# Performance work log

Hardware: AMD Instinct MI355X
Metric: run time of the kernel (lower is better)

The kernel has to match this reference:

```python
import jax, jax.numpy as jnp
import numpy as np

LEAKY_SLOPE = 0.01  # torch nn.LeakyReLU default


def leaky_relu(x):
    return jnp.where(x >= 0, x, LEAKY_SLOPE * x)


def rgcn_conv(x, edge_index, edge_type, w_rel, w_root, b_conv):
    # PyG RGCNConv: out = x @ W_root + b + sum_r mean_{edges of rel r into i}(x_src @ W_r)
    n = x.shape[0]
    src, dst = edge_index[0], edge_index[1]
    out = x @ w_root + b_conv
    num_rel = w_rel.shape[0]
    for r in range(num_rel):  # small fixed relation count
        mask = (edge_type == r)
        msg = x[src] @ w_rel[r]                      # [E, H]
        msg = jnp.where(mask[:, None], msg, 0.0)
        agg = jax.ops.segment_sum(msg, dst, num_segments=n)          # [N, H]
        cnt = jax.ops.segment_sum(mask.astype(x.dtype), dst, num_segments=n)
        out = out + agg / jnp.maximum(cnt, 1.0)[:, None]             # mean aggr
    return out


def setup_inputs() -> dict:
    key = jax.random.key(0)
    ks = jax.random.split(key, 10)
    N, E, D_IN, H, OUT, R = 50000, 600000, 768, 128, 3, 2
    s_in = 1.0 / np.sqrt(D_IN)
    s_h = 1.0 / np.sqrt(H)
    return {
        "feature": jax.random.normal(ks[0], (N, D_IN), dtype=jnp.float32),
        "edge_index": jax.random.randint(ks[1], (2, E), 0, N, dtype=jnp.int64),
        "edge_type": jax.random.randint(ks[2], (E,), 0, R, dtype=jnp.int64),
        "w_in": jax.random.uniform(ks[3], (D_IN, H), jnp.float32, -s_in, s_in),
        "b_in": jax.random.uniform(ks[4], (H,), jnp.float32, -s_in, s_in),
        "w_rel": jax.random.uniform(ks[5], (R, H, H), jnp.float32, -s_h, s_h),
        "w_root": jax.random.uniform(ks[6], (H, H), jnp.float32, -s_h, s_h),
        "b_conv": jnp.zeros((H,), jnp.float32),
        "w_out": jax.random.uniform(ks[7], (H, OUT), jnp.float32, -s_h, s_h),
        "b_out": jax.random.uniform(ks[8], (OUT,), jnp.float32, -s_h, s_h),
    }


def reference(feature, edge_index, edge_type, w_in, b_in, w_rel, w_root, b_conv, w_out, b_out):
    x = leaky_relu(feature @ w_in + b_in)
    # NOTE: original forward applies rgcn1 twice (shared weights); dropout is
    # identity at inference; rgcn2/linear_relu_output1 are unused.
    x = rgcn_conv(x, edge_index, edge_type, w_rel, w_root, b_conv)
    x = rgcn_conv(x, edge_index, edge_type, w_rel, w_root, b_conv)
    return x @ w_out + b_out
```

## Files before the change

### kernel.cpp

```cpp
#include <hip/hip_runtime.h>

#define H 128
#define CAP 64

typedef _Float16 f16x8 __attribute__((ext_vector_type(8)));
typedef _Float16 f16x4 __attribute__((ext_vector_type(4)));
typedef float    f32x4 __attribute__((ext_vector_type(4)));

__global__ __launch_bounds__(256) void hist_fill(const int* __restrict__ src,
    const int* __restrict__ dst, const int* __restrict__ et,
    int* __restrict__ cnt, int* __restrict__ elist, int E, int N)
{
    int e = blockIdx.x * 256 + threadIdx.x;
    if (e >= E) return;
    int s = src[e], d = dst[e], t = et[e];
    int b = t * N + d;
    int pos = atomicAdd(&cnt[b], 1);
    if (pos < CAP) elist[(size_t)b * CAP + pos] = s;
}

__global__ __launch_bounds__(256) void prep_w(const float* __restrict__ w_in,
    const float* __restrict__ w_root, const float* __restrict__ w_rel,
    _Float16* __restrict__ wInT, _Float16* __restrict__ wcatT, int K)
{
    int idx = blockIdx.x * 256 + threadIdx.x;
    int tot1 = K * H;
    if (idx < tot1) {
        int k = idx >> 7, c = idx & 127;
        int o = ((k >> 3) << 10) + (c << 3) + (k & 7);
        wInT[o] = (_Float16)w_in[idx];
    } else {
        int i2 = idx - tot1;
        if (i2 < H * 384) {
            int c = i2 / 384, k = i2 - c * 384;
            float v;
            if (k < 128)      v = w_root[(size_t)k * H + c];
            else if (k < 256) v = w_rel[(size_t)(k - 128) * H + c];
            else              v = w_rel[(size_t)H * H + (size_t)(k - 256) * H + c];
            wcatT[i2] = (_Float16)v;
        }
    }
}

__global__ __launch_bounds__(256) void prep_fin(const float* __restrict__ w_root,
    const float* __restrict__ w_rel, const float* __restrict__ b_conv,
    const float* __restrict__ w_out, const float* __restrict__ b_out,
    float* __restrict__ wfin, float* __restrict__ bfin, int OUT)
{
    int idx = blockIdx.x * 256 + threadIdx.x;
    if (idx < 3 * H) {
        int m = idx >> 7, k = idx & 127;
        const float* W = (m == 0) ? w_root : (w_rel + (size_t)(m - 1) * H * H);
        for (int c = 0; c < OUT; c++) {
            float s = 0.f;
            for (int j = 0; j < H; j++) s += W[(size_t)k * H + j] * w_out[(size_t)j * OUT + c];
            wfin[((size_t)m * H + k) * OUT + c] = s;
        }
    } else if (idx < 3 * H + OUT) {
        int c = idx - 3 * H;
        float s = b_out[c];
        for (int j = 0; j < H; j++) s += b_conv[j] * w_out[(size_t)j * OUT + c];
        bfin[c] = s;
    }
}

__global__ __launch_bounds__(256, 3) void gemm_big(const float* __restrict__ A,
    const _Float16* __restrict__ WP, const float* __restrict__ bias,
    _Float16* __restrict__ C16, int M, int K, int ldc)
{
    __shared__ _Float16 As[2][8192];

    const int tid = threadIdx.x;
    const int w   = tid >> 6;
    const int l   = tid & 63;
    const int l15 = l & 15;
    const int q   = l >> 4;
    const int brow = blockIdx.x * 64;
    const int wr   = w * 16;

    const int srow = wr + (l >> 5);
    const int sk4  = (l & 31) * 4;
    const int slot = (l & 31) >> 1;
    const int half = l & 1;

    const _Float16* bp = WP + ((size_t)q * H + l15) * 8;

    float bj[8];
#pragma unroll
    for (int j = 0; j < 8; j++) bj[j] = bias[j * 16 + l15];

    f32x4 acc[8];
    const f32x4 z4 = {0.f, 0.f, 0.f, 0.f};
#pragma unroll
    for (int j = 0; j < 8; j++) acc[j] = z4;

    const int chunks = K / 128;
    float4 st[8];

    {
        const float* apc = A + sk4;
#pragma unroll
        for (int i = 0; i < 8; i++) {
            int gr = brow + srow + i * 2; if (gr >= M) gr = M - 1;
            st[i] = *(const float4*)(apc + (size_t)gr * K);
        }
#pragma unroll
        for (int i = 0; i < 8; i++) {
            int row = srow + i * 2;
            int idx = slot * 512 + ((row ^ (slot & 7)) << 3) + half * 4;
            f16x4 v; v[0] = (_Float16)st[i].x; v[1] = (_Float16)st[i].y;
                     v[2] = (_Float16)st[i].z; v[3] = (_Float16)st[i].w;
            *(f16x4*)&As[0][idx] = v;
        }
    }
    __syncthreads();

    for (int c = 0; c < chunks; c++) {
        const bool more = (c + 1) < chunks;
        if (more) {
            const float* apc = A + (c + 1) * 128 + sk4;
#pragma unroll
            for (int i = 0; i < 8; i++) {
                int gr = brow + srow + i * 2; if (gr >= M) gr = M - 1;
                st[i] = *(const float4*)(apc + (size_t)gr * K);
            }
        }
        {
            const _Float16* __restrict__ buf = As[c & 1];
#pragma unroll
            for (int ks = 0; ks < 4; ks++) {
                const int sl = ks * 4 + q;
                f16x8 af = *(const f16x8*)&buf[sl * 512 + (((wr + l15) ^ (sl & 7)) << 3)];
                const _Float16* bks = bp + (size_t)(c * 4 + ks) * 4096;
                f16x8 bf[8];
#pragma unroll
                for (int j = 0; j < 8; j++) bf[j] = *(const f16x8*)(bks + j * 128);
#pragma unroll
                for (int j = 0; j < 8; j++)
                    acc[j] = __builtin_amdgcn_mfma_f32_16x16x32_f16(af, bf[j], acc[j], 0, 0, 0);
            }
        }
        if (more) {
            _Float16* __restrict__ buf = As[(c + 1) & 1];
#pragma unroll
            for (int i = 0; i < 8; i++) {
                int row = srow + i * 2;
                int idx = slot * 512 + ((row ^ (slot & 7)) << 3) + half * 4;
                f16x4 v; v[0] = (_Float16)st[i].x; v[1] = (_Float16)st[i].y;
                         v[2] = (_Float16)st[i].z; v[3] = (_Float16)st[i].w;
                *(f16x4*)&buf[idx] = v;
            }
        }
        __syncthreads();
    }

#pragma unroll
    for (int rg = 0; rg < 4; rg++) {
        int row = brow + wr + q * 4 + rg;
        if (row < M) {
#pragma unroll
            for (int j = 0; j < 8; j++) {
                float v = acc[j][rg] + bj[j];
                v = (v >= 0.f) ? v : 0.01f * v;
                C16[(size_t)row * ldc + j * 16 + l15] = (_Float16)v;
            }
        }
    }
}

template<int MODE>
__global__ __launch_bounds__(256) void gather_k(const _Float16* __restrict__ X,
    int ldx, _Float16* __restrict__ Mout, const int* __restrict__ elist,
    const int* __restrict__ cnt, int N,
    const float* __restrict__ wfin, const float* __restrict__ bfin,
    float* __restrict__ out)
{
    int wv = blockIdx.x * 4 + (threadIdx.x >> 6);
    int l  = threadIdx.x & 63;
    if (wv >= N) return;

    const int eo   = l >> 4;
    const int e2   = eo & 1;
    const int half = l >> 5;
    const int c8   = (l & 15) * 8;

    int dr = cnt[(size_t)half * N + wv];
    int d  = dr < CAP ? dr : CAP;
    float inv = dr > 0 ? 1.f / (float)dr : 0.f;
    const int* lst = elist + ((size_t)half * N + wv) * CAP;

    float acc[8];
#pragma unroll
    for (int j = 0; j < 8; j++) acc[j] = 0.f;

    const f16x8 zv = {};
    for (int p = e2; p < d; p += 8) {
        int p1 = p + 2, p2 = p + 4, p3 = p + 6;
        int s0 = lst[p];
        f16x8 v0 = *(const f16x8*)&X[(size_t)s0 * ldx + c8];
        f16x8 v1 = zv, v2 = zv, v3 = zv;
        if (p1 < d) { int s = lst[p1]; v1 = *(const f16x8*)&X[(size_t)s * ldx + c8]; }
        if (p2 < d) { int s = lst[p2]; v2 = *(const f16x8*)&X[(size_t)s * ldx + c8]; }
        if (p3 < d) { int s = lst[p3]; v3 = *(const f16x8*)&X[(size_t)s * ldx + c8]; }
#pragma unroll
        for (int j = 0; j < 8; j++)
            acc[j] += (float)v0[j] + (float)v1[j] + (float)v2[j] + (float)v3[j];
    }

#pragma unroll
    for (int j = 0; j < 8; j++) {
        acc[j] += __shfl_xor(acc[j], 16);
        acc[j] *= inv;
    }

    if (MODE == 0) {
        if (eo == 0) {
            f16x8 o;
#pragma unroll
            for (int j = 0; j < 8; j++) o[j] = (_Float16)acc[j];
            *(f16x8*)&Mout[(size_t)wv * 384 + 128 + c8] = o;
        } else if (eo == 2) {
            f16x8 o;
#pragma unroll
            for (int j = 0; j < 8; j++) o[j] = (_Float16)acc[j];
            *(f16x8*)&Mout[(size_t)wv * 384 + 256 + c8] = o;
        }
    } else {
        float p0 = 0.f, p1 = 0.f, p2 = 0.f;
        if (eo == 1) {
            f16x8 xv = *(const f16x8*)&X[(size_t)wv * ldx + c8];
#pragma unroll
            for (int j = 0; j < 8; j++) {
                float xf = (float)xv[j];
                const float* wr = wfin + (size_t)(c8 + j) * 3;
                p0 += xf * wr[0]; p1 += xf * wr[1]; p2 += xf * wr[2];
            }
        } else if (eo == 0 || eo == 2) {
            const float* wb = wfin + (size_t)(eo == 0 ? 1 : 2) * H * 3;
#pragma unroll
            for (int j = 0; j < 8; j++) {
                const float* wr = wb + (size_t)(c8 + j) * 3;
                p0 += acc[j] * wr[0]; p1 += acc[j] * wr[1]; p2 += acc[j] * wr[2];
            }
        }
#pragma unroll
        for (int off = 1; off <= 32; off <<= 1) {
            p0 += __shfl_xor(p0, off);
            p1 += __shfl_xor(p1, off);
            p2 += __shfl_xor(p2, off);
        }
        if (l == 0) {
            out[(size_t)wv * 3 + 0] = p0 + bfin[0];
            out[(size_t)wv * 3 + 1] = p1 + bfin[1];
            out[(size_t)wv * 3 + 2] = p2 + bfin[2];
        }
    }
}

__global__ __launch_bounds__(512) void gemm_cat(const _Float16* __restrict__ XC,
    const _Float16* __restrict__ WT, const float* __restrict__ bias,
    _Float16* __restrict__ X2, int M, int mtiles, int ldc)
{
    const int w   = threadIdx.x >> 6;
    const int l   = threadIdx.x & 63;
    const int l15 = l & 15;
    const int q   = l >> 4;
    const int col = w * 16 + l15;

    f16x8 bf[12];
    {
        const _Float16* wpp = WT + (size_t)col * 384 + q * 8;
#pragma unroll
        for (int c = 0; c < 12; c++) bf[c] = *(const f16x8*)(wpp + c * 32);
    }
    const float bj = bias[col];

    int t = blockIdx.x;
    if (t >= mtiles) return;
    f16x8 xf[12];
    {
        const _Float16* xp = XC + ((size_t)t * 16 + l15) * 384 + q * 8;
#pragma unroll
        for (int c = 0; c < 12; c++) xf[c] = *(const f16x8*)(xp + c * 32);
    }

    const f32x4 z4 = {0.f, 0.f, 0.f, 0.f};
    while (true) {
        int tn = t + gridDim.x;
        bool more = tn < mtiles;
        f16x8 xnf[12];
        if (more) {
            const _Float16* xp = XC + ((size_t)tn * 16 + l15) * 384 + q * 8;
#pragma unroll
            for (int c = 0; c < 12; c++) xnf[c] = *(const f16x8*)(xp + c * 32);
        }

        f32x4 a0 = z4;
#pragma unroll
        for (int c = 0; c < 12; c++)
            a0 = __builtin_amdgcn_mfma_f32_16x16x32_f16(xf[c], bf[c], a0, 0, 0, 0);

#pragma unroll
        for (int rg = 0; rg < 4; rg++) {
            int row = t * 16 + q * 4 + rg;
            if (row < M) X2[(size_t)row * ldc + col] = (_Float16)(a0[rg] + bj);
        }
        if (!more) break;
        t = tn;
#pragma unroll
        for (int c = 0; c < 12; c++) xf[c] = xnf[c];
    }
}

__global__ __launch_bounds__(256) void proj_generic(const _Float16* __restrict__ XC,
    const float* __restrict__ wfin, const float* __restrict__ bfin,
    float* __restrict__ out, int N, int OUT)
{
    int row = blockIdx.x * 4 + (threadIdx.x >> 6);
    int l = threadIdx.x & 63;
    if (row >= N) return;
    float xv[6];
#pragma unroll
    for (int i = 0; i < 6; i++) xv[i] = (float)XC[(size_t)row * 384 + l * 6 + i];
    for (int c = 0; c < OUT; c++) {
        float p = 0.f;
#pragma unroll
        for (int i = 0; i < 6; i++) p += xv[i] * wfin[(size_t)(l * 6 + i) * OUT + c];
        for (int off = 32; off > 0; off >>= 1) p += __shfl_down(p, off);
        if (l == 0) out[(size_t)row * OUT + c] = p + bfin[c];
    }
}

extern "C" void kernel_launch(void* const* d_in, const int* in_sizes, int n_in,
                              void* d_out, int out_size, void* d_ws, size_t ws_size,
                              hipStream_t stream) {
    const float* feature = (const float*)d_in[0];
    const int*   ei      = (const int*)d_in[1];
    const int*   et      = (const int*)d_in[2];
    const float* w_in    = (const float*)d_in[3];
    const float* b_in    = (const float*)d_in[4];
    const float* w_rel   = (const float*)d_in[5];
    const float* w_root  = (const float*)d_in[6];
    const float* b_conv  = (const float*)d_in[7];
    const float* w_out   = (const float*)d_in[8];
    const float* b_out   = (const float*)d_in[9];

    const int HH   = in_sizes[4];
    const int D_IN = in_sizes[3] / HH;
    const int N    = in_sizes[0] / D_IN;
    const int E    = in_sizes[1] / 2;
    const int OUT  = in_sizes[9];

    char* base = (char*)d_ws;
    _Float16* wInT  = (_Float16*)base;
    _Float16* wcatT = wInT + (size_t)D_IN * HH;
    _Float16* xc1   = wcatT + (size_t)HH * 384;
    _Float16* xc2   = xc1 + (size_t)N * 384;
    float* wfin     = (float*)(xc2 + (size_t)N * 384);
    float* bfin     = wfin + (size_t)3 * HH * (OUT > 0 ? OUT : 1);
    int* cnt        = (int*)(bfin + ((OUT + 3) & ~3));
    int* elist      = cnt + (size_t)2 * N;

    hipMemsetAsync(cnt, 0, sizeof(int) * (size_t)2 * N, stream);
    prep_w<<<(D_IN * HH + HH * 384 + 255) / 256, 256, 0, stream>>>(
        w_in, w_root, w_rel, wInT, wcatT, D_IN);
    prep_fin<<<2, 256, 0, stream>>>(w_root, w_rel, b_conv, w_out, b_out,
                                    wfin, bfin, OUT);
    hist_fill<<<(E + 255) / 256, 256, 0, stream>>>(ei, ei + E, et, cnt, elist, E, N);

    gemm_big<<<(N + 63) / 64, 256, 0, stream>>>(feature, wInT, b_in, xc1, N, D_IN, 384);

    const int mtiles  = (N + 15) / 16;
    const int gblocks = (N + 3) / 4;

    gather_k<0><<<gblocks, 256, 0, stream>>>(xc1, 384, xc1, elist, cnt, N,
                                             nullptr, nullptr, nullptr);
    if (OUT == 3) {
        gemm_cat<<<1024, 512, 0, stream>>>(xc1, wcatT, b_conv, xc2, N, mtiles, 128);
        gather_k<1><<<gblocks, 256, 0, stream>>>(xc2, 128, nullptr, elist, cnt, N,
                                                 wfin, bfin, (float*)d_out);
    } else {
        gemm_cat<<<1024, 512, 0, stream>>>(xc1, wcatT, b_conv, xc2, N, mtiles, 384);
        gather_k<0><<<gblocks, 256, 0, stream>>>(xc2, 384, xc2, elist, cnt, N,
                                                 nullptr, nullptr, nullptr);
        proj_generic<<<gblocks, 256, 0, stream>>>(xc2, wfin, bfin, (float*)d_out, N, OUT);
    }
}
```

Before: 449.2 us.

## Pre-convert features to fp16 and split concat buffer into separate arrays

Adds a standalone kernel that converts the fp32 feature matrix to fp16 so the input GEMM loads half-precision tiles directly with simpler staging. The 384-wide concatenated activation buffer is split into an N×128 node array and an N×256 aggregated-message array, with gemm_cat and the gather kernels updated to match. prep_fin is parallelised across output columns. The extra conversion pass adds a full read and write of the feature matrix, which may outweigh the savings in the GEMM's load path.

```diff
diff --git a/kernel.cpp b/kernel.cpp
--- a/kernel.cpp
+++ b/kernel.cpp
@@ -17,6 +17,23 @@
     int b = t * N + d;
     int pos = atomicAdd(&cnt[b], 1);
     if (pos < CAP) elist[(size_t)b * CAP + pos] = s;
+}
+
+__global__ __launch_bounds__(256) void cvt_feat(const float* __restrict__ A,
+    _Float16* __restrict__ A16, long long total8)
+{
+    long long i = (long long)blockIdx.x * 256 + threadIdx.x;
+    long long stride = (long long)gridDim.x * 256;
+    for (; i < total8; i += stride) {
+        float4 v0 = *(const float4*)(A + i * 8);
+        float4 v1 = *(const float4*)(A + i * 8 + 4);
+        f16x8 o;
+        o[0] = (_Float16)v0.x; o[1] = (_Float16)v0.y;
+        o[2] = (_Float16)v0.z; o[3] = (_Float16)v0.w;
+        o[4] = (_Float16)v1.x; o[5] = (_Float16)v1.y;
+        o[6] = (_Float16)v1.z; o[7] = (_Float16)v1.w;
+        *(f16x8*)(A16 + i * 8) = o;
+    }
 }
 
 __global__ __launch_bounds__(256) void prep_w(const float* __restrict__ w_in,
@@ -48,23 +65,24 @@
     float* __restrict__ wfin, float* __restrict__ bfin, int OUT)
 {
     int idx = blockIdx.x * 256 + threadIdx.x;
-    if (idx < 3 * H) {
-        int m = idx >> 7, k = idx & 127;
+    int nw = 3 * H * OUT;
+    if (idx < nw) {
+        int mk = idx / OUT, c = idx - mk * OUT;
+        int m = mk >> 7, k = mk & 127;
         const float* W = (m == 0) ? w_root : (w_rel + (size_t)(m - 1) * H * H);
-        for (int c = 0; c < OUT; c++) {
-            float s = 0.f;
-            for (int j = 0; j < H; j++) s += W[(size_t)k * H + j] * w_out[(size_t)j * OUT + c];
-            wfin[((size_t)m * H + k) * OUT + c] = s;
-        }
-    } else if (idx < 3 * H + OUT) {
-        int c = idx - 3 * H;
+        float s = 0.f;
+        for (int j = 0; j < H; j++)
+            s += W[(size_t)k * H + j] * w_out[(size_t)j * OUT + c];
+        wfin[(size_t)mk * OUT + c] = s;
+    } else if (idx < nw + OUT) {
+        int c = idx - nw;
         float s = b_out[c];
         for (int j = 0; j < H; j++) s += b_conv[j] * w_out[(size_t)j * OUT + c];
         bfin[c] = s;
     }
 }
 
-__global__ __launch_bounds__(256, 3) void gemm_big(const float* __restrict__ A,
+__global__ __launch_bounds__(256, 3) void gemm_big(const _Float16* __restrict__ A16,
     const _Float16* __restrict__ WP, const float* __restrict__ bias,
     _Float16* __restrict__ C16, int M, int K, int ldc)
 {
@@ -78,10 +96,8 @@
     const int brow = blockIdx.x * 64;
     const int wr   = w * 16;
 
-    const int srow = wr + (l >> 5);
-    const int sk4  = (l & 31) * 4;
-    const int slot = (l & 31) >> 1;
-    const int half = l & 1;
+    const int r4  = l >> 4;
+    const int c16 = l & 15;
 
     const _Float16* bp = WP + ((size_t)q * H + l15) * 8;
 
@@ -95,22 +111,19 @@
     for (int j = 0; j < 8; j++) acc[j] = z4;
 
     const int chunks = K / 128;
-    float4 st[8];
+    f16x8 st[4];
 
     {
-        const float* apc = A + sk4;
-#pragma unroll
-        for (int i = 0; i < 8; i++) {
-            int gr = brow + srow + i * 2; if (gr >= M) gr = M - 1;
-            st[i] = *(const float4*)(apc + (size_t)gr * K);
-        }
-#pragma unroll
-        for (int i = 0; i < 8; i++) {
-            int row = srow + i * 2;
-            int idx = slot * 512 + ((row ^ (slot & 7)) << 3) + half * 4;
-            f16x4 v; v[0] = (_Float16)st[i].x; v[1] = (_Float16)st[i].y;
-                     v[2] = (_Float16)st[i].z; v[3] = (_Float16)st[i].w;
-            *(f16x4*)&As[0][idx] = v;
+        const _Float16* apc = A16 + c16 * 8;
+#pragma unroll
+        for (int i = 0; i < 4; i++) {
+            int gr = brow + wr + r4 + i * 4; if (gr >= M) gr = M - 1;
+            st[i] = *(const f16x8*)(apc + (size_t)gr * K);
+        }
+#pragma unroll
+        for (int i = 0; i < 4; i++) {
+            int row = wr + r4 + i * 4;
+            *(f16x8*)&As[0][c16 * 512 + ((row ^ (c16 & 7)) << 3)] = st[i];
         }
     }
     __syncthreads();
@@ -118,11 +131,11 @@
     for (int c = 0; c < chunks; c++) {
         const bool more = (c + 1) < chunks;
         if (more) {
-            const float* apc = A + (c + 1) * 128 + sk4;
-#pragma unroll
-            for (int i = 0; i < 8; i++) {
-                int gr = brow + srow + i * 2; if (gr >= M) gr = M - 1;
-                st[i] = *(const float4*)(apc + (size_t)gr * K);
+            const _Float16* apc = A16 + (c + 1) * 128 + c16 * 8;
+#pragma unroll
+            for (int i = 0; i < 4; i++) {
+                int gr = brow + wr + r4 + i * 4; if (gr >= M) gr = M - 1;
+                st[i] = *(const f16x8*)(apc + (size_t)gr * K);
             }
         }
         {
@@ -143,12 +156,9 @@
         if (more) {
             _Float16* __restrict__ buf = As[(c + 1) & 1];
 #pragma unroll
-            for (int i = 0; i < 8; i++) {
-                int row = srow + i * 2;
-                int idx = slot * 512 + ((row ^ (slot & 7)) << 3) + half * 4;
-                f16x4 v; v[0] = (_Float16)st[i].x; v[1] = (_Float16)st[i].y;
-                         v[2] = (_Float16)st[i].z; v[3] = (_Float16)st[i].w;
-                *(f16x4*)&buf[idx] = v;
+            for (int i = 0; i < 4; i++) {
+                int row = wr + r4 + i * 4;
+                *(f16x8*)&buf[c16 * 512 + ((row ^ (c16 & 7)) << 3)] = st[i];
             }
         }
         __syncthreads();
@@ -214,16 +224,11 @@
     }
 
     if (MODE == 0) {
-        if (eo == 0) {
+        if (eo == 0 || eo == 2) {
             f16x8 o;
 #pragma unroll
             for (int j = 0; j < 8; j++) o[j] = (_Float16)acc[j];
-            *(f16x8*)&Mout[(size_t)wv * 384 + 128 + c8] = o;
-        } else if (eo == 2) {
-            f16x8 o;
-#pragma unroll
-            for (int j = 0; j < 8; j++) o[j] = (_Float16)acc[j];
-            *(f16x8*)&Mout[(size_t)wv * 384 + 256 + c8] = o;
+            *(f16x8*)&Mout[(size_t)wv * 256 + half * 128 + c8] = o;
         }
     } else {
         float p0 = 0.f, p1 = 0.f, p2 = 0.f;
@@ -257,9 +262,9 @@
     }
 }
 
-__global__ __launch_bounds__(512) void gemm_cat(const _Float16* __restrict__ XC,
-    const _Float16* __restrict__ WT, const float* __restrict__ bias,
-    _Float16* __restrict__ X2, int M, int mtiles, int ldc)
+__global__ __launch_bounds__(512) void gemm_cat(const _Float16* __restrict__ X1,
+    const _Float16* __restrict__ Mt, const _Float16* __restrict__ WT,
+    const float* __restrict__ bias, _Float16* __restrict__ X2, int M, int mtiles)
 {
     const int w   = threadIdx.x >> 6;
     const int l   = threadIdx.x & 63;
@@ -279,9 +284,12 @@
     if (t >= mtiles) return;
     f16x8 xf[12];
     {
-        const _Float16* xp = XC + ((size_t)t * 16 + l15) * 384 + q * 8;
-#pragma unroll
-        for (int c = 0; c < 12; c++) xf[c] = *(const f16x8*)(xp + c * 32);
+        const _Float16* xp = X1 + ((size_t)t * 16 + l15) * 128 + q * 8;
+        const _Float16* mp = Mt + ((size_t)t * 16 + l15) * 256 + q * 8;
+#pragma unroll
+        for (int c = 0; c < 4; c++) xf[c] = *(const f16x8*)(xp + c * 32);
+#pragma unroll
+        for (int c = 4; c < 12; c++) xf[c] = *(const f16x8*)(mp + (c - 4) * 32);
     }
 
     const f32x4 z4 = {0.f, 0.f, 0.f, 0.f};
@@ -290,9 +298,12 @@
         bool more = tn < mtiles;
         f16x8 xnf[12];
         if (more) {
-            const _Float16* xp = XC + ((size_t)tn * 16 + l15) * 384 + q * 8;
-#pragma unroll
-            for (int c = 0; c < 12; c++) xnf[c] = *(const f16x8*)(xp + c * 32);
+            const _Float16* xp = X1 + ((size_t)tn * 16 + l15) * 128 + q * 8;
+            const _Float16* mp = Mt + ((size_t)tn * 16 + l15) * 256 + q * 8;
+#pragma unroll
+            for (int c = 0; c < 4; c++) xnf[c] = *(const f16x8*)(xp + c * 32);
+#pragma unroll
+            for (int c = 4; c < 12; c++) xnf[c] = *(const f16x8*)(mp + (c - 4) * 32);
         }
 
         f32x4 a0 = z4;
@@ -303,7 +314,7 @@
 #pragma unroll
         for (int rg = 0; rg < 4; rg++) {
             int row = t * 16 + q * 4 + rg;
-            if (row < M) X2[(size_t)row * ldc + col] = (_Float16)(a0[rg] + bj);
+            if (row < M) X2[(size_t)row * 128 + col] = (_Float16)(a0[rg] + bj);
         }
         if (!more) break;
         t = tn;
@@ -312,16 +323,20 @@
     }
 }
 
-__global__ __launch_bounds__(256) void proj_generic(const _Float16* __restrict__ XC,
-    const float* __restrict__ wfin, const float* __restrict__ bfin,
-    float* __restrict__ out, int N, int OUT)
+__global__ __launch_bounds__(256) void proj_generic(const _Float16* __restrict__ X2,
+    const _Float16* __restrict__ Mt, const float* __restrict__ wfin,
+    const float* __restrict__ bfin, float* __restrict__ out, int N, int OUT)
 {
     int row = blockIdx.x * 4 + (threadIdx.x >> 6);
     int l = threadIdx.x & 63;
     if (row >= N) return;
     float xv[6];
 #pragma unroll
-    for (int i = 0; i < 6; i++) xv[i] = (float)XC[(size_t)row * 384 + l * 6 + i];
+    for (int i = 0; i < 6; i++) {
+        int k = l * 6 + i;
+        xv[i] = (k < 128) ? (float)X2[(size_t)row * 128 + k]
+                          : (float)Mt[(size_t)row * 256 + (k - 128)];
+    }
     for (int c = 0; c < OUT; c++) {
         float p = 0.f;
 #pragma unroll
@@ -352,11 +367,13 @@
     const int OUT  = in_sizes[9];
 
     char* base = (char*)d_ws;
-    _Float16* wInT  = (_Float16*)base;
+    _Float16* A16   = (_Float16*)base;
+    _Float16* wInT  = A16 + (size_t)N * D_IN;
     _Float16* wcatT = wInT + (size_t)D_IN * HH;
-    _Float16* xc1   = wcatT + (size_t)HH * 384;
-    _Float16* xc2   = xc1 + (size_t)N * 384;
-    float* wfin     = (float*)(xc2 + (size_t)N * 384);
+    _Float16* X1    = wcatT + (size_t)HH * 384;
+    _Float16* X2    = X1 + (size_t)N * HH;
+    _Float16* Mt    = X2 + (size_t)N * HH;
+    float* wfin     = (float*)(Mt + (size_t)N * 256);
     float* bfin     = wfin + (size_t)3 * HH * (OUT > 0 ? OUT : 1);
     int* cnt        = (int*)(bfin + ((OUT + 3) & ~3));
     int* elist      = cnt + (size_t)2 * N;
@@ -364,25 +381,27 @@
     hipMemsetAsync(cnt, 0, sizeof(int) * (size_t)2 * N, stream);
     prep_w<<<(D_IN * HH + HH * 384 + 255) / 256, 256, 0, stream>>>(
         w_in, w_root, w_rel, wInT, wcatT, D_IN);
-    prep_fin<<<2, 256, 0, stream>>>(w_root, w_rel, b_conv, w_out, b_out,
-                                    wfin, bfin, OUT);
+    prep_fin<<<(3 * HH * OUT + OUT + 255) / 256, 256, 0, stream>>>(
+        w_root, w_rel, b_conv, w_out, b_out, wfin, bfin, OUT);
     hist_fill<<<(E + 255) / 256, 256, 0, stream>>>(ei, ei + E, et, cnt, elist, E, N);
 
-    gemm_big<<<(N + 63) / 64, 256, 0, stream>>>(feature, wInT, b_in, xc1, N, D_IN, 384);
+    long long total8 = (long long)N * D_IN / 8;
+    cvt_feat<<<2048, 256, 0, stream>>>(feature, A16, total8);
+    gemm_big<<<(N + 63) / 64, 256, 0, stream>>>(A16, wInT, b_in, X1, N, D_IN, HH);
 
     const int mtiles  = (N + 15) / 16;
     const int gblocks = (N + 3) / 4;
 
-    gather_k<0><<<gblocks, 256, 0, stream>>>(xc1, 384, xc1, elist, cnt, N,
+    gather_k<0><<<gblocks, 256, 0, stream>>>(X1, 128, Mt, elist, cnt, N,
                                              nullptr, nullptr, nullptr);
+    gemm_cat<<<1024, 512, 0, stream>>>(X1, Mt, wcatT, b_conv, X2, N, mtiles);
     if (OUT == 3) {
-        gemm_cat<<<1024, 512, 0, stream>>>(xc1, wcatT, b_conv, xc2, N, mtiles, 128);
-        gather_k<1><<<gblocks, 256, 0, stream>>>(xc2, 128, nullptr, elist, cnt, N,
+        gather_k<1><<<gblocks, 256, 0, stream>>>(X2, 128, nullptr, elist, cnt, N,
                                                  wfin, bfin, (float*)d_out);
     } else {
-        gemm_cat<<<1024, 512, 0, stream>>>(xc1, wcatT, b_conv, xc2, N, mtiles, 384);
-        gather_k<0><<<gblocks, 256, 0, stream>>>(xc2, 384, xc2, elist, cnt, N,
+        gather_k<0><<<gblocks, 256, 0, stream>>>(X2, 128, Mt, elist, cnt, N,
                                                  nullptr, nullptr, nullptr);
-        proj_generic<<<gblocks, 256, 0, stream>>>(xc2, wfin, bfin, (float*)d_out, N, OUT);
-    }
-}
+        proj_generic<<<gblocks, 256, 0, stream>>>(X2, Mt, wfin, bfin,
+                                                  (float*)d_out, N, OUT);
+    }
+}
```

New measurement: 462.1 us. 1.03x slower.
